# Performance work log

Hardware: AMD Instinct MI355X
Metric: run time of the kernel (lower is better)

Reference implementation:

```python
import jax, jax.numpy as jnp
import numpy as np

BIT_DEPTH = 8  # feature squeezing

def setup_inputs() -> dict:
    key = jax.random.key(0)
    ks = jax.random.split(key, 8)
    B, C, H, W = 8, 256, 64, 64
    Cq = C // 8
    x = jax.random.normal(ks[0], (B, C, H, W), dtype=jnp.float32)
    # 1x1 conv weights stored as [out, in] (kernel dims squeezed)
    wq = jax.random.normal(ks[1], (Cq, C), dtype=jnp.float32) * 0.05
    bq = jax.random.normal(ks[2], (Cq,), dtype=jnp.float32) * 0.05
    wk = jax.random.normal(ks[3], (Cq, C), dtype=jnp.float32) * 0.05
    bk = jax.random.normal(ks[4], (Cq,), dtype=jnp.float32) * 0.05
    wv = jax.random.normal(ks[5], (C, C), dtype=jnp.float32) * 0.05
    bv = jax.random.normal(ks[6], (C,), dtype=jnp.float32) * 0.05
    gamma = jax.random.normal(ks[7], (1,), dtype=jnp.float32) * 0.1
    return {"x": x, "wq": wq, "bq": bq, "wk": wk, "bk": bk, "wv": wv, "bv": bv, "gamma": gamma}

def reference(x, wq, bq, wk, bk, wv, bv, gamma):
    B, C, H, W = x.shape
    N = H * W
    xf = x.reshape(B, C, N)  # flatten spatial
    # 1x1 convs == per-pixel linear projections
    q = jnp.einsum('bcn,oc->bon', xf, wq) + bq[None, :, None]   # [B, C/8, N]
    k = jnp.einsum('bcn,oc->bon', xf, wk) + bk[None, :, None]   # [B, C/8, N]
    v = jnp.einsum('bcn,oc->bon', xf, wv) + bv[None, :, None]   # [B, C, N]
    energy = jnp.einsum('bcn,bcm->bnm', q, k)                   # [B, N, N] (no scaling, as in source)
    attn = jax.nn.softmax(energy, axis=-1)
    out = jnp.einsum('bcm,bnm->bcn', v, attn).reshape(B, C, H, W)
    out = gamma[0] * out + out               # gamma-scaled residual of attention output
    scale = jnp.float32(2 ** BIT_DEPTH)
    return jnp.floor(out * scale) / scale    # feature squeezing (bit_depth=8)
```

## Files before the change

kernel.cpp:

```cpp
#include <hip/hip_runtime.h>
#include <math.h>

namespace {
constexpr int BB = 8;
constexpr int CH = 256;
constexpr int CQ = 32;
constexpr int NN = 4096;
}

typedef float f32x4 __attribute__((ext_vector_type(4)));
typedef short bf16x8 __attribute__((ext_vector_type(8)));
typedef unsigned short us8 __attribute__((ext_vector_type(8)));

#define MFMA16(a, b, c) __builtin_amdgcn_mfma_f32_16x16x32_bf16(a, b, c, 0, 0, 0)

__device__ __forceinline__ unsigned short f2bf(float x) {
    unsigned int u = __float_as_uint(x);
    u += 0x7fffu + ((u >> 16) & 1u);
    return (unsigned short)(u >> 16);
}
__device__ __forceinline__ float bf2f(unsigned short h) {
    return __uint_as_float(((unsigned int)h) << 16);
}
__device__ __forceinline__ void gload16(const void* g, void* l) {
    __builtin_amdgcn_global_load_lds(
        (const __attribute__((address_space(1))) unsigned int*)g,
        (__attribute__((address_space(3))) unsigned int*)l, 16, 0, 0);
}

__global__ __launch_bounds__(256) void wsplit_kernel(
    const float* __restrict__ wq, const float* __restrict__ wk,
    const float* __restrict__ wv,
    unsigned short* __restrict__ wh, unsigned short* __restrict__ wl)
{
    int idx = blockIdx.x * 256 + threadIdx.x;
    float v;
    if (idx < 8192)       v = wq[idx];
    else if (idx < 16384) v = wk[idx - 8192];
    else                  v = wv[idx - 16384];
    unsigned short hi = f2bf(v);
    wh[idx] = hi;
    wl[idx] = f2bf(v - bf2f(hi));
}

__global__ __launch_bounds__(256) void transpose_kernel(
    const float* __restrict__ x,
    unsigned short* __restrict__ xh, unsigned short* __restrict__ xl)
{
    __shared__ float xf[64 * 68];
    __shared__ unsigned short hs[64 * 80];
    __shared__ unsigned short ls[64 * 80];
    const int t  = threadIdx.x;
    const int b  = blockIdx.x >> 8;
    const int tl = blockIdx.x & 255;
    const int c0 = (tl >> 6) * 64;
    const int n0 = (tl & 63) * 64;

    #pragma unroll
    for (int i = 0; i < 4; ++i) {
        int idx = i * 256 + t;
        int c = idx >> 4, nf = idx & 15;
        float4 v4 = *(const float4*)(x + ((size_t)(b * 256 + c0 + c)) * NN + n0 + nf * 4);
        *(float4*)(xf + c * 68 + nf * 4) = v4;
    }
    __syncthreads();

    const int n = t & 63;
    #pragma unroll
    for (int loop = 0; loop < 2; ++loop) {
        int chunk = (t >> 6) + 4 * loop;
        us8 h8, l8;
        #pragma unroll
        for (int j = 0; j < 8; ++j) {
            float v = xf[(chunk * 8 + j) * 68 + n];
            unsigned short hi = f2bf(v);
            h8[j] = hi;
            l8[j] = f2bf(v - bf2f(hi));
        }
        *(us8*)(hs + n * 80 + chunk * 8) = h8;
        *(us8*)(ls + n * 80 + chunk * 8) = l8;
    }
    __syncthreads();

    {
        int rn = t >> 2, piece = t & 3;
        size_t grow = ((size_t)(b * NN + n0 + rn)) * 256 + c0 + piece * 16;
        *(f32x4*)((float*)0 + 0);
        *(us8*)(xh + grow)     = *(const us8*)(hs + rn * 80 + piece * 16);
        *(us8*)(xh + grow + 8) = *(const us8*)(hs + rn * 80 + piece * 16 + 8);
        *(us8*)(xl + grow)     = *(const us8*)(ls + rn * 80 + piece * 16);
        *(us8*)(xl + grow + 8) = *(const us8*)(ls + rn * 80 + piece * 16 + 8);
    }
}

#define PJ_XL 32768
#define PJ_VE 16384
__global__ __launch_bounds__(256, 2) void proj_kernel(
    const unsigned short* __restrict__ xh, const unsigned short* __restrict__ xl,
    const unsigned short* __restrict__ wh, const unsigned short* __restrict__ wl,
    const float* __restrict__ bq, const float* __restrict__ bk,
    const float* __restrict__ bv,
    unsigned short* __restrict__ qh, unsigned short* __restrict__ ql,
    unsigned short* __restrict__ kh, unsigned short* __restrict__ kl,
    unsigned short* __restrict__ vt)
{
    __shared__ __align__(16) unsigned char smem[65536];
    const int t    = threadIdx.x;
    const int lane = t & 63;
    const int w    = t >> 6;
    const int l16  = lane & 15;
    const int quad = lane >> 4;
    const int b    = blockIdx.x >> 6;
    const int n0   = (blockIdx.x & 63) << 6;

    const unsigned char* xhB = (const unsigned char*)(xh + ((size_t)b * NN + n0) * 256);
    const unsigned char* xlB = (const unsigned char*)(xl + ((size_t)b * NN + n0) * 256);
    #pragma unroll
    for (int j = 0; j < 8; ++j) {
        int idx = j * 256 + t;
        int r = idx >> 5, cl = idx & 31;
        int cg = cl ^ (r & 7);
        gload16(xhB + (size_t)r * 512 + cg * 16, smem + idx * 16);
        gload16(xlB + (size_t)r * 512 + cg * 16, smem + PJ_XL + idx * 16);
    }
    __syncthreads();

    f32x4 acc[5][4] = {};
    #pragma unroll 1
    for (int kc = 0; kc < 8; ++kc) {
        bf16x8 ah[5], al[5];
        #pragma unroll
        for (int i = 0; i < 5; ++i) {
            int och = (w * 5 + i) * 16 + l16;
            ah[i] = *(const bf16x8*)(wh + och * 256 + kc * 32 + quad * 8);
            al[i] = *(const bf16x8*)(wl + och * 256 + kc * 32 + quad * 8);
        }
        #pragma unroll
        for (int nt = 0; nt < 4; ++nt) {
            int roff = (nt * 16 + l16) * 512 + (((kc * 4 + quad) ^ (l16 & 7)) * 16);
            bf16x8 bh = *(const bf16x8*)(smem + roff);
            bf16x8 bl = *(const bf16x8*)(smem + PJ_XL + roff);
            #pragma unroll
            for (int i = 0; i < 5; ++i) {
                acc[i][nt] = MFMA16(ah[i], bh, acc[i][nt]);
                acc[i][nt] = MFMA16(al[i], bh, acc[i][nt]);
                acc[i][nt] = MFMA16(ah[i], bl, acc[i][nt]);
            }
        }
    }
    __syncthreads();

    #pragma unroll
    for (int i = 0; i < 5; ++i) {
        int tile = w * 5 + i;
        if (tile < 4) {
            #pragma unroll
            for (int r = 0; r < 4; ++r) {
                int och = tile * 16 + quad * 4 + r;
                float bias = (och < 32) ? bq[och] : bk[och - 32];
                int arr = (och < 32) ? 0 : 2;
                int oq = och & 31;
                #pragma unroll
                for (int nt = 0; nt < 4; ++nt) {
                    float val = acc[i][nt][r] + bias;
                    unsigned short hi = f2bf(val);
                    unsigned short lo = f2bf(val - bf2f(hi));
                    *(unsigned short*)(smem + arr * 4096 + (nt * 16 + l16) * 64 + oq * 2) = hi;
                    *(unsigned short*)(smem + (arr + 1) * 4096 + (nt * 16 + l16) * 64 + oq * 2) = lo;
                }
            }
        } else {
            #pragma unroll
            for (int r = 0; r < 4; ++r) {
                int voch = tile * 16 + quad * 4 + r - 64;
                float bias = bv[voch];
                #pragma unroll
                for (int nt = 0; nt < 4; ++nt) {
                    *(unsigned short*)(smem + PJ_VE + voch * 136 + (nt * 16 + l16) * 2)
                        = f2bf(acc[i][nt][r] + bias);
                }
            }
        }
    }
    __syncthreads();

    {
        unsigned short* dsts[4] = { qh, ql, kh, kl };
        int arr = t >> 6, n = t & 63;
        unsigned short* dst = dsts[arr] + ((size_t)b * NN + n0 + n) * 32;
        #pragma unroll
        for (int i = 0; i < 4; ++i)
            *(us8*)(dst + i * 8) = *(const us8*)(smem + arr * 4096 + n * 64 + i * 16);
    }
    #pragma unroll
    for (int p = 0; p < 4; ++p) {
        int voch = p * 64 + (t >> 2), piece = t & 3;
        unsigned short* dst = vt + ((size_t)b * CH + voch) * NN + n0 + piece * 16;
        *(us8*)(dst)     = *(const us8*)(smem + PJ_VE + voch * 136 + piece * 32);
        *(us8*)(dst + 8) = *(const us8*)(smem + PJ_VE + voch * 136 + piece * 32 + 16);
    }
}

#define A_KH 0
#define A_KL 4096
#define A_V  8192
#define A_P  40960
#define A_SM 50176

__global__ __launch_bounds__(256, 2) void attn_kernel(
    const unsigned short* __restrict__ qh, const unsigned short* __restrict__ ql,
    const unsigned short* __restrict__ kh, const unsigned short* __restrict__ kl,
    const unsigned short* __restrict__ vt, const float* __restrict__ gptr,
    float* __restrict__ out)
{
    __shared__ __align__(16) unsigned char smem[51200];
    const int t    = threadIdx.x;
    const int lane = t & 63;
    const int w    = t >> 6;
    const int l16  = lane & 15;
    const int quad = lane >> 4;
    const int b    = blockIdx.x & 7;
    const int n0   = (blockIdx.x >> 3) << 6;

    bf16x8 qhA[4], qlA[4];
    #pragma unroll
    for (int qt = 0; qt < 4; ++qt) {
        size_t row = (size_t)b * NN + n0 + qt * 16 + l16;
        qhA[qt] = *(const bf16x8*)(qh + row * 32 + quad * 8);
        qlA[qt] = *(const bf16x8*)(ql + row * 32 + quad * 8);
    }

    const unsigned char* khB = (const unsigned char*)(kh + (size_t)b * NN * 32);
    const unsigned char* klB = (const unsigned char*)(kl + (size_t)b * NN * 32);
    const unsigned char* vtB = (const unsigned char*)(vt + (size_t)b * CH * NN);

    f32x4 acc[4][4] = {};
    float S[4][4] = {};

    #pragma unroll 1
    for (int tile = 0; tile < 64; ++tile) {
        const int m0 = tile * 64;
        __syncthreads();
        {
            int r = t >> 2, cl = t & 3;
            int cg = cl ^ ((r >> 1) & 3);
            gload16(khB + (size_t)(m0 + r) * 64 + cg * 16, smem + A_KH + t * 16);
            gload16(klB + (size_t)(m0 + r) * 64 + cg * 16, smem + A_KL + t * 16);
        }
        #pragma unroll
        for (int j = 0; j < 8; ++j) {
            int idx = j * 256 + t;
            int r = idx >> 3, cl = idx & 7;
            int cg = cl ^ (r & 7);
            gload16(vtB + (size_t)r * 8192 + (size_t)m0 * 2 + cg * 16,
                    smem + A_V + idx * 16);
        }
        __syncthreads();

        {
            int row = w * 16 + l16;
            int koff = row * 64 + ((quad ^ ((l16 >> 1) & 3)) * 16);
            bf16x8 bh = *(const bf16x8*)(smem + A_KH + koff);
            bf16x8 bl = *(const bf16x8*)(smem + A_KL + koff);
            #pragma unroll
            for (int qt = 0; qt < 4; ++qt) {
                f32x4 e = { 0.f, 0.f, 0.f, 0.f };
                e = MFMA16(qhA[qt], bh, e);
                e = MFMA16(qlA[qt], bh, e);
                e = MFMA16(qhA[qt], bl, e);
                #pragma unroll
                for (int r = 0; r < 4; ++r) {
                    float p = __expf(e[r]);
                    unsigned short pb = f2bf(p);
                    S[qt][r] += bf2f(pb);
                    *(unsigned short*)(smem + A_P + (qt * 16 + quad * 4 + r) * 144
                                            + (w * 16 + l16) * 2) = pb;
                }
            }
        }
        __syncthreads();

        #pragma unroll
        for (int ks = 0; ks < 2; ++ks) {
            bf16x8 af[4], bfr[4];
            #pragma unroll
            for (int qt = 0; qt < 4; ++qt)
                af[qt] = *(const bf16x8*)(smem + A_P + (qt * 16 + l16) * 144
                                               + ks * 64 + quad * 16);
            #pragma unroll
            for (int ct = 0; ct < 4; ++ct) {
                int row = w * 64 + ct * 16 + l16;
                int ch = (ks * 4 + quad) ^ (l16 & 7);
                bfr[ct] = *(const bf16x8*)(smem + A_V + row * 128 + ch * 16);
            }
            #pragma unroll
            for (int qt = 0; qt < 4; ++qt)
                #pragma unroll
                for (int ct = 0; ct < 4; ++ct)
                    acc[qt][ct] = MFMA16(af[qt], bfr[ct], acc[qt][ct]);
        }
    }

    #pragma unroll
    for (int mask = 1; mask <= 8; mask <<= 1)
        #pragma unroll
        for (int qt = 0; qt < 4; ++qt)
            #pragma unroll
            for (int r = 0; r < 4; ++r)
                S[qt][r] += __shfl_xor(S[qt][r], mask);
    float* SM = (float*)(smem + A_SM);
    if (l16 == 0) {
        #pragma unroll
        for (int qt = 0; qt < 4; ++qt)
            #pragma unroll
            for (int r = 0; r < 4; ++r)
                SM[w * 64 + qt * 16 + quad * 4 + r] = S[qt][r];
    }
    __syncthreads();

    const float g1 = 1.f + gptr[0];
    float* ob = out + (size_t)b * CH * NN;
    #pragma unroll
    for (int qt = 0; qt < 4; ++qt) {
        float is[4];
        #pragma unroll
        for (int r = 0; r < 4; ++r) {
            int qi = qt * 16 + quad * 4 + r;
            float Sf = SM[qi] + SM[64 + qi] + SM[128 + qi] + SM[192 + qi];
            is[r] = g1 / Sf;
        }
        #pragma unroll
        for (int ct = 0; ct < 4; ++ct) {
            float4 o4;
            o4.x = floorf(acc[qt][ct][0] * is[0] * 256.f) * 0.00390625f;
            o4.y = floorf(acc[qt][ct][1] * is[1] * 256.f) * 0.00390625f;
            o4.z = floorf(acc[qt][ct][2] * is[2] * 256.f) * 0.00390625f;
            o4.w = floorf(acc[qt][ct][3] * is[3] * 256.f) * 0.00390625f;
            *(float4*)(ob + (size_t)(w * 64 + ct * 16 + l16) * NN
                          + n0 + qt * 16 + quad * 4) = o4;
        }
    }
}

extern "C" void kernel_launch(void* const* d_in, const int* in_sizes, int n_in,
                              void* d_out, int out_size, void* d_ws, size_t ws_size,
                              hipStream_t stream) {
    const float* x  = (const float*)d_in[0];
    const float* wq = (const float*)d_in[1];
    const float* bq = (const float*)d_in[2];
    const float* wk = (const float*)d_in[3];
    const float* bk = (const float*)d_in[4];
    const float* wv = (const float*)d_in[5];
    const float* bv = (const float*)d_in[6];
    const float* gm = (const float*)d_in[7];
    float* out = (float*)d_out;

    unsigned short* ws = (unsigned short*)d_ws;
    const size_t XSZ = (size_t)BB * NN * 256;
    const size_t WSZ = 320 * 256;
    const size_t QSZ = (size_t)BB * NN * 32;
    unsigned short* xh = ws;
    unsigned short* xl = xh + XSZ;
    unsigned short* wh = xl + XSZ;
    unsigned short* wl = wh + WSZ;
    unsigned short* qh = wl + WSZ;
    unsigned short* ql = qh + QSZ;
    unsigned short* kh = ql + QSZ;
    unsigned short* kl = kh + QSZ;
    unsigned short* vt = kl + QSZ;

    wsplit_kernel<<<320, 256, 0, stream>>>(wq, wk, wv, wh, wl);
    transpose_kernel<<<2048, 256, 0, stream>>>(x, xh, xl);
    proj_kernel<<<512, 256, 0, stream>>>(xh, xl, wh, wl, bq, bk, bv,
                                         qh, ql, kh, kl, vt);
    attn_kernel<<<512, 256, 0, stream>>>(qh, ql, kh, kl, vt, gm, out);
}
```

Baseline: 244.6 us.

## Fuse transpose into projection and software-pipeline attention with smaller key tiles

The separate transpose/split kernel is removed: the projection kernel now loads fp32 x directly into shared memory, splits it into hi/lo bf16 and stores it in a swizzled layout, which avoids a full round trip of xh/xl through global memory. The attention kernel is restructured to use 32-key tiles with a triple-buffered K/V prefetch and double-buffered P, so each wave owns 16 query rows. The P·V MFMAs for the previous tile overlap with the QK/exp work of the current one, and there is one barrier per iteration instead of three. The cost is more shared memory per block (about 80 KB and 70 KB), which may limit occupancy, and twice as many loop iterations.

```diff
diff --git a/kernel.cpp b/kernel.cpp
--- a/kernel.cpp
+++ b/kernel.cpp
@@ -4,7 +4,6 @@
 namespace {
 constexpr int BB = 8;
 constexpr int CH = 256;
-constexpr int CQ = 32;
 constexpr int NN = 4096;
 }
 
@@ -43,60 +42,14 @@
     wl[idx] = f2bf(v - bf2f(hi));
 }
 
-__global__ __launch_bounds__(256) void transpose_kernel(
+#define PJ_XH 0
+#define PJ_XL 32768
+#define PJ_ST 65536
+#define PJ_QK 65536
+#define PJ_VE 0
+
+__global__ __launch_bounds__(256, 2) void proj_kernel(
     const float* __restrict__ x,
-    unsigned short* __restrict__ xh, unsigned short* __restrict__ xl)
-{
-    __shared__ float xf[64 * 68];
-    __shared__ unsigned short hs[64 * 80];
-    __shared__ unsigned short ls[64 * 80];
-    const int t  = threadIdx.x;
-    const int b  = blockIdx.x >> 8;
-    const int tl = blockIdx.x & 255;
-    const int c0 = (tl >> 6) * 64;
-    const int n0 = (tl & 63) * 64;
-
-    #pragma unroll
-    for (int i = 0; i < 4; ++i) {
-        int idx = i * 256 + t;
-        int c = idx >> 4, nf = idx & 15;
-        float4 v4 = *(const float4*)(x + ((size_t)(b * 256 + c0 + c)) * NN + n0 + nf * 4);
-        *(float4*)(xf + c * 68 + nf * 4) = v4;
-    }
-    __syncthreads();
-
-    const int n = t & 63;
-    #pragma unroll
-    for (int loop = 0; loop < 2; ++loop) {
-        int chunk = (t >> 6) + 4 * loop;
-        us8 h8, l8;
-        #pragma unroll
-        for (int j = 0; j < 8; ++j) {
-            float v = xf[(chunk * 8 + j) * 68 + n];
-            unsigned short hi = f2bf(v);
-            h8[j] = hi;
-            l8[j] = f2bf(v - bf2f(hi));
-        }
-        *(us8*)(hs + n * 80 + chunk * 8) = h8;
-        *(us8*)(ls + n * 80 + chunk * 8) = l8;
-    }
-    __syncthreads();
-
-    {
-        int rn = t >> 2, piece = t & 3;
-        size_t grow = ((size_t)(b * NN + n0 + rn)) * 256 + c0 + piece * 16;
-        *(f32x4*)((float*)0 + 0);
-        *(us8*)(xh + grow)     = *(const us8*)(hs + rn * 80 + piece * 16);
-        *(us8*)(xh + grow + 8) = *(const us8*)(hs + rn * 80 + piece * 16 + 8);
-        *(us8*)(xl + grow)     = *(const us8*)(ls + rn * 80 + piece * 16);
-        *(us8*)(xl + grow + 8) = *(const us8*)(ls + rn * 80 + piece * 16 + 8);
-    }
-}
-
-#define PJ_XL 32768
-#define PJ_VE 16384
-__global__ __launch_bounds__(256, 2) void proj_kernel(
-    const unsigned short* __restrict__ xh, const unsigned short* __restrict__ xl,
     const unsigned short* __restrict__ wh, const unsigned short* __restrict__ wl,
     const float* __restrict__ bq, const float* __restrict__ bk,
     const float* __restrict__ bv,
@@ -104,7 +57,7 @@
     unsigned short* __restrict__ kh, unsigned short* __restrict__ kl,
     unsigned short* __restrict__ vt)
 {
-    __shared__ __align__(16) unsigned char smem[65536];
+    __shared__ __align__(16) unsigned char smem[81920];
     const int t    = threadIdx.x;
     const int lane = t & 63;
     const int w    = t >> 6;
@@ -113,15 +66,34 @@
     const int b    = blockIdx.x >> 6;
     const int n0   = (blockIdx.x & 63) << 6;
 
-    const unsigned char* xhB = (const unsigned char*)(xh + ((size_t)b * NN + n0) * 256);
-    const unsigned char* xlB = (const unsigned char*)(xl + ((size_t)b * NN + n0) * 256);
-    #pragma unroll
-    for (int j = 0; j < 8; ++j) {
-        int idx = j * 256 + t;
-        int r = idx >> 5, cl = idx & 31;
-        int cg = cl ^ (r & 7);
-        gload16(xhB + (size_t)r * 512 + cg * 16, smem + idx * 16);
-        gload16(xlB + (size_t)r * 512 + cg * 16, smem + PJ_XL + idx * 16);
+    const unsigned char* xB = (const unsigned char*)x + ((size_t)b * 256 * NN + n0) * 4;
+    const int n = t & 63;
+    #pragma unroll 1
+    for (int cg = 0; cg < 4; ++cg) {
+        __syncthreads();
+        #pragma unroll
+        for (int j = 0; j < 4; ++j) {
+            int idx = j * 256 + t;
+            int cr = idx >> 4, nch = idx & 15;
+            gload16(xB + (size_t)(cg * 64 + cr) * NN * 4 + nch * 16,
+                    smem + PJ_ST + idx * 16);
+        }
+        __syncthreads();
+        #pragma unroll
+        for (int it = 0; it < 2; ++it) {
+            int o = (t >> 6) + 4 * it;
+            us8 h8, l8;
+            #pragma unroll
+            for (int j = 0; j < 8; ++j) {
+                float v = *(const float*)(smem + PJ_ST + (o * 8 + j) * 256 + n * 4);
+                unsigned short hi = f2bf(v);
+                h8[j] = hi;
+                l8[j] = f2bf(v - bf2f(hi));
+            }
+            int pch = (cg * 8 + o) ^ (n & 7);
+            *(us8*)(smem + PJ_XH + n * 512 + pch * 16) = h8;
+            *(us8*)(smem + PJ_XL + n * 512 + pch * 16) = l8;
+        }
     }
     __syncthreads();
 
@@ -138,7 +110,7 @@
         #pragma unroll
         for (int nt = 0; nt < 4; ++nt) {
             int roff = (nt * 16 + l16) * 512 + (((kc * 4 + quad) ^ (l16 & 7)) * 16);
-            bf16x8 bh = *(const bf16x8*)(smem + roff);
+            bf16x8 bh = *(const bf16x8*)(smem + PJ_XH + roff);
             bf16x8 bl = *(const bf16x8*)(smem + PJ_XL + roff);
             #pragma unroll
             for (int i = 0; i < 5; ++i) {
@@ -165,8 +137,8 @@
                     float val = acc[i][nt][r] + bias;
                     unsigned short hi = f2bf(val);
                     unsigned short lo = f2bf(val - bf2f(hi));
-                    *(unsigned short*)(smem + arr * 4096 + (nt * 16 + l16) * 64 + oq * 2) = hi;
-                    *(unsigned short*)(smem + (arr + 1) * 4096 + (nt * 16 + l16) * 64 + oq * 2) = lo;
+                    *(unsigned short*)(smem + PJ_QK + arr * 4096 + (nt * 16 + l16) * 64 + oq * 2) = hi;
+                    *(unsigned short*)(smem + PJ_QK + (arr + 1) * 4096 + (nt * 16 + l16) * 64 + oq * 2) = lo;
                 }
             }
         } else {
@@ -186,11 +158,11 @@
 
     {
         unsigned short* dsts[4] = { qh, ql, kh, kl };
-        int arr = t >> 6, n = t & 63;
-        unsigned short* dst = dsts[arr] + ((size_t)b * NN + n0 + n) * 32;
+        int arr = t >> 6, rn = t & 63;
+        unsigned short* dst = dsts[arr] + ((size_t)b * NN + n0 + rn) * 32;
         #pragma unroll
         for (int i = 0; i < 4; ++i)
-            *(us8*)(dst + i * 8) = *(const us8*)(smem + arr * 4096 + n * 64 + i * 16);
+            *(us8*)(dst + i * 8) = *(const us8*)(smem + PJ_QK + arr * 4096 + rn * 64 + i * 16);
     }
     #pragma unroll
     for (int p = 0; p < 4; ++p) {
@@ -201,11 +173,10 @@
     }
 }
 
-#define A_KH 0
-#define A_KL 4096
-#define A_V  8192
-#define A_P  40960
-#define A_SM 50176
+#define AV_OFF 0
+#define AK_OFF 49152
+#define AP_OFF 61440
+#define AS_OFF 71680
 
 __global__ __launch_bounds__(256, 2) void attn_kernel(
     const unsigned short* __restrict__ qh, const unsigned short* __restrict__ ql,
@@ -213,7 +184,7 @@
     const unsigned short* __restrict__ vt, const float* __restrict__ gptr,
     float* __restrict__ out)
 {
-    __shared__ __align__(16) unsigned char smem[51200];
+    __shared__ __align__(16) unsigned char smem[71936];
     const int t    = threadIdx.x;
     const int lane = t & 63;
     const int w    = t >> 6;
@@ -222,99 +193,126 @@
     const int b    = blockIdx.x & 7;
     const int n0   = (blockIdx.x >> 3) << 6;
 
-    bf16x8 qhA[4], qlA[4];
-    #pragma unroll
-    for (int qt = 0; qt < 4; ++qt) {
-        size_t row = (size_t)b * NN + n0 + qt * 16 + l16;
-        qhA[qt] = *(const bf16x8*)(qh + row * 32 + quad * 8);
-        qlA[qt] = *(const bf16x8*)(ql + row * 32 + quad * 8);
-    }
-
-    const unsigned char* khB = (const unsigned char*)(kh + (size_t)b * NN * 32);
-    const unsigned char* klB = (const unsigned char*)(kl + (size_t)b * NN * 32);
-    const unsigned char* vtB = (const unsigned char*)(vt + (size_t)b * CH * NN);
+    const size_t qrow = (size_t)b * NN + n0 + w * 16 + l16;
+    const bf16x8 qhA = *(const bf16x8*)(qh + qrow * 32 + quad * 8);
+    const bf16x8 qlA = *(const bf16x8*)(ql + qrow * 32 + quad * 8);
+
+    const unsigned char* ksrc;
+    int kdst;
+    {
+        int c = t & 127, kr = c >> 2, cl = c & 3;
+        int cg = cl ^ ((kr >> 1) & 3);
+        ksrc = (const unsigned char*)((t < 128) ? kh : kl)
+             + (size_t)b * NN * 64 + (size_t)kr * 64 + cg * 16;
+        kdst = AK_OFF + (t >> 7) * 2048 + c * 16;
+    }
+    const unsigned char* vsrc;
+    {
+        int vr = t >> 2, cl = t & 3;
+        int cg = cl ^ (vr & 3);
+        vsrc = (const unsigned char*)vt + (size_t)b * CH * NN * 2
+             + (size_t)vr * 8192 + cg * 16;
+    }
 
     f32x4 acc[4][4] = {};
-    float S[4][4] = {};
+    float S[4] = {};
+
+    {
+        gload16(ksrc, smem + kdst);
+        unsigned char* vd = smem + AV_OFF + t * 16;
+        gload16(vsrc,           vd);
+        gload16(vsrc + 524288,  vd + 4096);
+        gload16(vsrc + 1048576, vd + 8192);
+        gload16(vsrc + 1572864, vd + 12288);
+    }
+    __syncthreads();
+
+    int bprv = 2, bcur = 0, bnxt = 1, pcur = 0;
+    const int koffbase = (quad ^ ((l16 >> 1) & 3)) * 16;
+    const int voffbase = (quad ^ (l16 & 3)) * 16;
 
     #pragma unroll 1
-    for (int tile = 0; tile < 64; ++tile) {
-        const int m0 = tile * 64;
-        __syncthreads();
+    for (int r = 0; r < 128; ++r) {
+        if (r < 127) {
+            const unsigned char* ks = ksrc + (size_t)(r + 1) * 2048;
+            gload16(ks, smem + bnxt * 4096 + kdst);
+            const unsigned char* vs = vsrc + (size_t)(r + 1) * 64;
+            unsigned char* vd = smem + AV_OFF + bnxt * 16384 + t * 16;
+            gload16(vs,           vd);
+            gload16(vs + 524288,  vd + 4096);
+            gload16(vs + 1048576, vd + 8192);
+            gload16(vs + 1572864, vd + 12288);
+        }
         {
-            int r = t >> 2, cl = t & 3;
-            int cg = cl ^ ((r >> 1) & 3);
-            gload16(khB + (size_t)(m0 + r) * 64 + cg * 16, smem + A_KH + t * 16);
-            gload16(klB + (size_t)(m0 + r) * 64 + cg * 16, smem + A_KL + t * 16);
-        }
-        #pragma unroll
-        for (int j = 0; j < 8; ++j) {
-            int idx = j * 256 + t;
-            int r = idx >> 3, cl = idx & 7;
-            int cg = cl ^ (r & 7);
-            gload16(vtB + (size_t)r * 8192 + (size_t)m0 * 2 + cg * 16,
-                    smem + A_V + idx * 16);
-        }
-        __syncthreads();
-
-        {
-            int row = w * 16 + l16;
-            int koff = row * 64 + ((quad ^ ((l16 >> 1) & 3)) * 16);
-            bf16x8 bh = *(const bf16x8*)(smem + A_KH + koff);
-            bf16x8 bl = *(const bf16x8*)(smem + A_KL + koff);
-            #pragma unroll
-            for (int qt = 0; qt < 4; ++qt) {
+            const unsigned char* kb = smem + AK_OFF + bcur * 4096;
+            unsigned char* pb = smem + AP_OFF + pcur * 5120;
+            #pragma unroll
+            for (int kt = 0; kt < 2; ++kt) {
+                int ko = (kt * 16 + l16) * 64 + koffbase;
+                bf16x8 bh = *(const bf16x8*)(kb + ko);
+                bf16x8 bl = *(const bf16x8*)(kb + 2048 + ko);
                 f32x4 e = { 0.f, 0.f, 0.f, 0.f };
-                e = MFMA16(qhA[qt], bh, e);
-                e = MFMA16(qlA[qt], bh, e);
-                e = MFMA16(qhA[qt], bl, e);
+                e = MFMA16(qhA, bh, e);
+                e = MFMA16(qlA, bh, e);
+                e = MFMA16(qhA, bl, e);
                 #pragma unroll
-                for (int r = 0; r < 4; ++r) {
-                    float p = __expf(e[r]);
-                    unsigned short pb = f2bf(p);
-                    S[qt][r] += bf2f(pb);
-                    *(unsigned short*)(smem + A_P + (qt * 16 + quad * 4 + r) * 144
-                                            + (w * 16 + l16) * 2) = pb;
+                for (int rr = 0; rr < 4; ++rr) {
+                    float p = __expf(e[rr]);
+                    unsigned short pv16 = f2bf(p);
+                    S[rr] += bf2f(pv16);
+                    *(unsigned short*)(pb + (w * 16 + quad * 4 + rr) * 80
+                                          + (kt * 16 + l16) * 2) = pv16;
                 }
             }
         }
-        __syncthreads();
-
-        #pragma unroll
-        for (int ks = 0; ks < 2; ++ks) {
-            bf16x8 af[4], bfr[4];
+        if (r > 0) {
+            const unsigned char* pp = smem + AP_OFF + (pcur ^ 1) * 5120;
+            const unsigned char* vb = smem + AV_OFF + bprv * 16384;
+            bf16x8 aP[4], bV[4];
             #pragma unroll
             for (int qt = 0; qt < 4; ++qt)
-                af[qt] = *(const bf16x8*)(smem + A_P + (qt * 16 + l16) * 144
-                                               + ks * 64 + quad * 16);
-            #pragma unroll
-            for (int ct = 0; ct < 4; ++ct) {
-                int row = w * 64 + ct * 16 + l16;
-                int ch = (ks * 4 + quad) ^ (l16 & 7);
-                bfr[ct] = *(const bf16x8*)(smem + A_V + row * 128 + ch * 16);
-            }
+                aP[qt] = *(const bf16x8*)(pp + (qt * 16 + l16) * 80 + quad * 16);
+            #pragma unroll
+            for (int ct = 0; ct < 4; ++ct)
+                bV[ct] = *(const bf16x8*)(vb + (w * 64 + ct * 16 + l16) * 64 + voffbase);
             #pragma unroll
             for (int qt = 0; qt < 4; ++qt)
                 #pragma unroll
                 for (int ct = 0; ct < 4; ++ct)
-                    acc[qt][ct] = MFMA16(af[qt], bfr[ct], acc[qt][ct]);
-        }
+                    acc[qt][ct] = MFMA16(aP[qt], bV[ct], acc[qt][ct]);
+        }
+        __syncthreads();
+        bprv = bcur; bcur = bnxt; ++bnxt; if (bnxt == 3) bnxt = 0;
+        pcur ^= 1;
+    }
+    {
+        const unsigned char* pp = smem + AP_OFF + (pcur ^ 1) * 5120;
+        const unsigned char* vb = smem + AV_OFF + bprv * 16384;
+        bf16x8 aP[4], bV[4];
+        #pragma unroll
+        for (int qt = 0; qt < 4; ++qt)
+            aP[qt] = *(const bf16x8*)(pp + (qt * 16 + l16) * 80 + quad * 16);
+        #pragma unroll
+        for (int ct = 0; ct < 4; ++ct)
+            bV[ct] = *(const bf16x8*)(vb + (w * 64 + ct * 16 + l16) * 64 + voffbase);
+        #pragma unroll
+        for (int qt = 0; qt < 4; ++qt)
+            #pragma unroll
+            for (int ct = 0; ct < 4; ++ct)
+                acc[qt][ct] = MFMA16(aP[qt], bV[ct], acc[qt][ct]);
     }
 
     #pragma unroll
     for (int mask = 1; mask <= 8; mask <<= 1)
         #pragma unroll
-        for (int qt = 0; qt < 4; ++qt)
-            #pragma unroll
-            for (int r = 0; r < 4; ++r)
-                S[qt][r] += __shfl_xor(S[qt][r], mask);
-    float* SM = (float*)(smem + A_SM);
+        for (int rr = 0; rr < 4; ++rr)
+            S[rr] += __shfl_xor(S[rr], mask);
+    float* SM = (float*)(smem + AS_OFF);
+    __syncthreads();
     if (l16 == 0) {
         #pragma unroll
-        for (int qt = 0; qt < 4; ++qt)
-            #pragma unroll
-            for (int r = 0; r < 4; ++r)
-                SM[w * 64 + qt * 16 + quad * 4 + r] = S[qt][r];
+        for (int rr = 0; rr < 4; ++rr)
+            SM[w * 16 + quad * 4 + rr] = S[rr];
     }
     __syncthreads();
 
@@ -324,11 +322,8 @@
     for (int qt = 0; qt < 4; ++qt) {
         float is[4];
         #pragma unroll
-        for (int r = 0; r < 4; ++r) {
-            int qi = qt * 16 + quad * 4 + r;
-            float Sf = SM[qi] + SM[64 + qi] + SM[128 + qi] + SM[192 + qi];
-            is[r] = g1 / Sf;
-        }
+        for (int rr = 0; rr < 4; ++rr)
+            is[rr] = g1 / SM[qt * 16 + quad * 4 + rr];
         #pragma unroll
         for (int ct = 0; ct < 4; ++ct) {
             float4 o4;
@@ -356,12 +351,9 @@
     float* out = (float*)d_out;
 
     unsigned short* ws = (unsigned short*)d_ws;
-    const size_t XSZ = (size_t)BB * NN * 256;
     const size_t WSZ = 320 * 256;
     const size_t QSZ = (size_t)BB * NN * 32;
-    unsigned short* xh = ws;
-    unsigned short* xl = xh + XSZ;
-    unsigned short* wh = xl + XSZ;
+    unsigned short* wh = ws;
     unsigned short* wl = wh + WSZ;
     unsigned short* qh = wl + WSZ;
     unsigned short* ql = qh + QSZ;
@@ -370,8 +362,7 @@
     unsigned short* vt = kl + QSZ;
 
     wsplit_kernel<<<320, 256, 0, stream>>>(wq, wk, wv, wh, wl);
-    transpose_kernel<<<2048, 256, 0, stream>>>(x, xh, xl);
-    proj_kernel<<<512, 256, 0, stream>>>(xh, xl, wh, wl, bq, bk, bv,
+    proj_kernel<<<512, 256, 0, stream>>>(x, wh, wl, bq, bk, bv,
                                          qh, ql, kh, kl, vt);
     attn_kernel<<<512, 256, 0, stream>>>(qh, ql, kh, kl, vt, gm, out);
 }
```

New measurement: 246.9 us. No clear change (+0.9%).
